# Kernel optimization log

Measured on AMD Instinct MI355X. Metric: run time of the kernel, lower is better.

The kernel has to match this reference:

```python
import jax, jax.numpy as jnp
import numpy as np

N, M, D = 1024, 1024, 512


def setup_inputs() -> dict:
    key = jax.random.key(0)
    ks = jax.random.split(key, 12)
    s = 1.0 / np.sqrt(D)
    return {
        "q": jax.random.normal(ks[0], (N, D), jnp.float32),
        "k": jax.random.normal(ks[1], (M, D), jnp.float32),
        "v": jax.random.normal(ks[2], (M, D), jnp.float32),
        "mask": jax.random.randint(ks[3], (N, M), 0, 2) > 0,
        "Wq": jax.random.normal(ks[4], (D, D), jnp.float32) * s,
        "bq": jax.random.normal(ks[5], (D,), jnp.float32) * s,
        "Wk": jax.random.normal(ks[6], (D, D), jnp.float32) * s,
        "bk": jax.random.normal(ks[7], (D,), jnp.float32) * s,
        "Wv": jax.random.normal(ks[8], (D, D), jnp.float32) * s,
        "bv": jax.random.normal(ks[9], (D,), jnp.float32) * s,
        "Ww": jax.random.normal(ks[10], (D,), jnp.float32) * s,
        "bw": jax.random.normal(ks[11], (1,), jnp.float32) * s,
    }


def reference(q, k, v, mask, Wq, bq, Wk, bk, Wv, bv, Ww, bw):
    # Linear projections (torch Linear: x @ W.T + b)
    qp = q @ Wq.T + bq  # [N, D]
    kp = k @ Wk.T + bk  # [M, D]
    vp = v @ Wv.T + bv  # [M, D]
    # Bahdanau additive score: W(tanh(q_n + k_m)) -> [N, M]
    h = jnp.tanh(qp[:, None, :] + kp[None, :, :])  # [N, M, D]
    scores = jnp.einsum('nmd,d->nm', h, Ww) + bw[0]
    scores = jnp.where(mask, scores, jnp.float32(-1000000.0))
    attn = jax.nn.softmax(scores, axis=1)  # softmax over M (dim 1)
    context = jnp.einsum('nm,md->nd', attn, vp)  # [N, D]
    return context
```

## Files before the change

### kernel.cpp

```cpp
#include <hip/hip_runtime.h>
#include <hip/hip_bf16.h>
#include <float.h>


#define NROWS 1024
#define DDIM  512
#define MDIM  1024

typedef __attribute__((ext_vector_type(8))) short s8v;
typedef __attribute__((ext_vector_type(4))) float f4v;
typedef __attribute__((ext_vector_type(2))) float v2f;

__device__ __forceinline__ ushort f2bf(float f) {
    unsigned u = __float_as_uint(f);
    u = u + 0x7FFFu + ((u >> 16) & 1u);
    return (ushort)(u >> 16);
}
__device__ __forceinline__ float bf2f(ushort h) {
    return __uint_as_float(((unsigned)h) << 16);
}

__device__ __forceinline__ void load_lds16(const float* g, float* l) {
    __builtin_amdgcn_global_load_lds(
        (const __attribute__((address_space(1))) void*)g,
        (__attribute__((address_space(3))) void*)l, 16, 0, 0);
}

__global__ __launch_bounds__(256) void proj_gemm(
    const float* __restrict__ q, const float* __restrict__ kk_,
    const float* __restrict__ v,
    const float* __restrict__ Wq, const float* __restrict__ bq,
    const float* __restrict__ Wk, const float* __restrict__ bk,
    const float* __restrict__ Wv, const float* __restrict__ bv,
    float* __restrict__ eq, float* __restrict__ ekT,
    ushort* __restrict__ vph, ushort* __restrict__ vpl,
    float* __restrict__ rsum, float CS)
{
    __shared__ ushort Ah[4096], Al[4096], Bh[4096], Bl[4096];

    const float* A; const float* B; const float* bias;
    int biasRow;
    if (blockIdx.z == 0)      { A = q;   B = Wq;  bias = bq; biasRow = 0; }
    else if (blockIdx.z == 1) { A = Wk;  B = kk_; bias = bk; biasRow = 1; }
    else                      { A = Wv;  B = v;   bias = bv; biasRow = 1; }

    const int bi = (blockIdx.z == 0) ? blockIdx.x : blockIdx.y;
    const int bj = (blockIdx.z == 0) ? blockIdx.y : blockIdx.x;

    const int t    = threadIdx.x;
    const int lane = t & 63;
    const int w    = t >> 6;
    const int lm   = lane & 15;
    const int lq   = lane >> 4;
    const int i0   = bi * 64;
    const int j0   = bj * 64;
    const int mh   = (w >> 1) * 32;
    const int nh   = (w & 1) * 32;

    if (blockIdx.z == 0 && bi == 0 && bj == 0) {
        float4 zz = {0.f, 0.f, 0.f, 0.f};
        *(float4*)&rsum[t * 4] = zz;
    }

    f4v acc[2][2] = {{{0.f,0.f,0.f,0.f},{0.f,0.f,0.f,0.f}},
                     {{0.f,0.f,0.f,0.f},{0.f,0.f,0.f,0.f}}};
    float4 pa[4], pb[4];

    const int sr = t >> 4, sc4 = t & 15;
#pragma unroll
    for (int p = 0; p < 4; ++p) {
        int r = sr + p * 16;
        pa[p] = *(const float4*)&A[(size_t)(i0 + r) * DDIM + sc4 * 4];
        pb[p] = *(const float4*)&B[(size_t)(j0 + r) * DDIM + sc4 * 4];
    }

    for (int kc = 0; kc < 8; ++kc) {
        __syncthreads();
#pragma unroll
        for (int p = 0; p < 4; ++p) {
            int r = sr + p * 16;
            int ad = r * 64 + (((sc4 >> 1) ^ (r & 7)) << 3) + (sc4 & 1) * 4;
            float af[4] = {pa[p].x, pa[p].y, pa[p].z, pa[p].w};
            float bf[4] = {pb[p].x, pb[p].y, pb[p].z, pb[p].w};
            ushort ah4[4], al4[4], bh4[4], bl4[4];
#pragma unroll
            for (int e = 0; e < 4; ++e) {
                ah4[e] = f2bf(af[e]); al4[e] = f2bf(af[e] - bf2f(ah4[e]));
                bh4[e] = f2bf(bf[e]); bl4[e] = f2bf(bf[e] - bf2f(bh4[e]));
            }
            *(ushort4*)&Ah[ad] = *(ushort4*)ah4;
            *(ushort4*)&Al[ad] = *(ushort4*)al4;
            *(ushort4*)&Bh[ad] = *(ushort4*)bh4;
            *(ushort4*)&Bl[ad] = *(ushort4*)bl4;
        }
        __syncthreads();
        if (kc < 7) {
            const int k0 = (kc + 1) * 64;
#pragma unroll
            for (int p = 0; p < 4; ++p) {
                int r = sr + p * 16;
                pa[p] = *(const float4*)&A[(size_t)(i0 + r) * DDIM + k0 + sc4 * 4];
                pb[p] = *(const float4*)&B[(size_t)(j0 + r) * DDIM + k0 + sc4 * 4];
            }
        }
#pragma unroll
        for (int ks = 0; ks < 2; ++ks) {
            const int kb = ks * 4 + lq;
            s8v afh[2], afl[2], bfh[2], bfl[2];
#pragma unroll
            for (int g = 0; g < 2; ++g) {
                int ra = mh + g * 16 + lm;
                int rb = nh + g * 16 + lm;
                int aa = ra * 64 + ((kb ^ (ra & 7)) << 3);
                int ab = rb * 64 + ((kb ^ (rb & 7)) << 3);
                afh[g] = *(const s8v*)&Ah[aa];
                afl[g] = *(const s8v*)&Al[aa];
                bfh[g] = *(const s8v*)&Bh[ab];
                bfl[g] = *(const s8v*)&Bl[ab];
            }
#pragma unroll
            for (int mi = 0; mi < 2; ++mi)
#pragma unroll
                for (int ni = 0; ni < 2; ++ni) {
                    acc[mi][ni] = __builtin_amdgcn_mfma_f32_16x16x32_bf16(
                        afh[mi], bfh[ni], acc[mi][ni], 0, 0, 0);
                    acc[mi][ni] = __builtin_amdgcn_mfma_f32_16x16x32_bf16(
                        afh[mi], bfl[ni], acc[mi][ni], 0, 0, 0);
                    acc[mi][ni] = __builtin_amdgcn_mfma_f32_16x16x32_bf16(
                        afl[mi], bfh[ni], acc[mi][ni], 0, 0, 0);
                }
        }
    }

    const float CLAMP = 8192.0f;
#pragma unroll
    for (int mi = 0; mi < 2; ++mi) {
#pragma unroll
        for (int ni = 0; ni < 2; ++ni) {
#pragma unroll
            for (int p = 0; p < 4; ++p) {
                int row = i0 + mh + mi * 16 + lq * 4 + p;
                int col = j0 + nh + ni * 16 + lm;
                float val = acc[mi][ni][p] + (biasRow ? bias[row] : bias[col]);
                if (blockIdx.z == 0) {
                    eq[(size_t)row * 512 + col] =
                        fminf(__builtin_amdgcn_exp2f(val * CS), CLAMP);
                } else if (blockIdx.z == 1) {
                    ekT[(size_t)row * 1024 + col] =
                        fminf(__builtin_amdgcn_exp2f(val * CS), CLAMP);
                } else {
                    ushort h = f2bf(val);
                    vph[(size_t)row * 1024 + col] = h;
                    vpl[(size_t)row * 1024 + col] = f2bf(val - bf2f(h));
                }
            }
        }
    }
}

#define DCH  32
#define SMCH 128
__global__ __launch_bounds__(256) void score_kernel(const float* __restrict__ eq,
                                                    const float* __restrict__ ekT,
                                                    const float* __restrict__ Ww,
                                                    const int* __restrict__ mask,
                                                    ushort* __restrict__ Ph,
                                                    ushort* __restrict__ Pl,
                                                    float* __restrict__ rsum)
{
    __shared__ __align__(16) float ks[DCH * SMCH];
    __shared__ __align__(16) float es[16 * DCH];
    __shared__ __align__(16) float wws[DCH];
    const int t    = threadIdx.x;
    const int lane = t & 63;
    const int w    = t >> 6;
    const int m0   = blockIdx.x * SMCH;
    const int n0   = blockIdx.y * 16;

    v2f acc[4] = {};
    const v2f one2 = {1.f, 1.f};

    for (int d0 = 0; d0 < DDIM; d0 += DCH) {
        __syncthreads();
#pragma unroll
        for (int i = 0; i < 4; ++i) {
            int r2 = w * 8 + i * 2;
            const float* g = ekT + (size_t)(d0 + r2 + (lane >> 5)) * MDIM
                             + m0 + (lane & 31) * 4;
            load_lds16(g, &ks[r2 * SMCH]);
        }
#pragma unroll
        for (int p = 0; p < 2; ++p) {
            int idx = t + p * 256;
            int nl = idx >> 5, dd = idx & 31;
            es[nl * DCH + dd] = eq[(size_t)(n0 + nl) * DDIM + d0 + dd];
        }
        if (t < DCH) wws[t] = Ww[d0 + t];
        __syncthreads();

#pragma unroll
        for (int dq = 0; dq < DCH; dq += 4) {
            v2f k0 = *(const v2f*)&ks[(dq + 0) * SMCH + lane * 2];
            v2f k1 = *(const v2f*)&ks[(dq + 1) * SMCH + lane * 2];
            v2f k2 = *(const v2f*)&ks[(dq + 2) * SMCH + lane * 2];
            v2f k3 = *(const v2f*)&ks[(dq + 3) * SMCH + lane * 2];
            float4 wg = *(const float4*)&wws[dq];
#pragma unroll
            for (int nn = 0; nn < 4; ++nn) {
                float4 eg = *(const float4*)&es[(w * 4 + nn) * DCH + dq];
                v2f A0 = __builtin_elementwise_fma(k0, (v2f){eg.x, eg.x}, one2);
                v2f A1 = __builtin_elementwise_fma(k1, (v2f){eg.y, eg.y}, one2);
                v2f A2 = __builtin_elementwise_fma(k2, (v2f){eg.z, eg.z}, one2);
                v2f A3 = __builtin_elementwise_fma(k3, (v2f){eg.w, eg.w}, one2);
                v2f n01 = __builtin_elementwise_fma((v2f){wg.y, wg.y}, A0,
                                                    (v2f){wg.x, wg.x} * A1);
                v2f d01 = A0 * A1;
                v2f n23 = __builtin_elementwise_fma((v2f){wg.w, wg.w}, A2,
                                                    (v2f){wg.z, wg.z} * A3);
                v2f d23 = A2 * A3;
                v2f num = __builtin_elementwise_fma(n01, d23, n23 * d01);
                v2f den = d01 * d23;
                v2f r = {__builtin_amdgcn_rcpf(den.x), __builtin_amdgcn_rcpf(den.y)};
                acc[nn] = __builtin_elementwise_fma(num, r, acc[nn]);
            }
        }
    }

    const float C2 = -2.8853900817779268f;
    const int m = m0 + lane * 2;
#pragma unroll
    for (int nn = 0; nn < 4; ++nn) {
        int n = n0 + w * 4 + nn;
        int2 mk = *(const int2*)&mask[(size_t)n * MDIM + m];
        float o0 = mk.x ? __builtin_amdgcn_exp2f(acc[nn].x * C2) : 0.f;
        float o1 = mk.y ? __builtin_amdgcn_exp2f(acc[nn].y * C2) : 0.f;
        ushort h0 = f2bf(o0), h1 = f2bf(o1);
        ushort l0 = f2bf(o0 - bf2f(h0)), l1 = f2bf(o1 - bf2f(h1));
        ushort2 hh = {h0, h1}, ll = {l0, l1};
        *(ushort2*)&Ph[(size_t)n * MDIM + m] = hh;
        *(ushort2*)&Pl[(size_t)n * MDIM + m] = ll;
        float rs = o0 + o1;
#pragma unroll
        for (int off = 32; off; off >>= 1) rs += __shfl_xor(rs, off);
        if (lane == 0) atomicAdd(&rsum[n], rs);
    }
}

__global__ __launch_bounds__(256) void ctx_gemm(const ushort* __restrict__ Ph,
                                                const ushort* __restrict__ Pl,
                                                const ushort* __restrict__ vph,
                                                const ushort* __restrict__ vpl,
                                                const float* __restrict__ rsum,
                                                float* __restrict__ out)
{
    const int t    = threadIdx.x;
    const int lane = t & 63;
    const int w    = t >> 6;
    const int lm   = lane & 15;
    const int lq   = lane >> 4;
    const int d0   = blockIdx.x * 64 + w * 16;
    const int n0   = blockIdx.y * 16;

    const ushort* pAh = Ph  + (size_t)(n0 + lm) * MDIM + lq * 8;
    const ushort* pAl = Pl  + (size_t)(n0 + lm) * MDIM + lq * 8;
    const ushort* pBh = vph + (size_t)(d0 + lm) * MDIM + lq * 8;
    const ushort* pBl = vpl + (size_t)(d0 + lm) * MDIM + lq * 8;

    f4v acc = {0.f, 0.f, 0.f, 0.f};
#pragma unroll 4
    for (int m0 = 0; m0 < MDIM; m0 += 32) {
        s8v ah = *(const s8v*)(pAh + m0);
        s8v al = *(const s8v*)(pAl + m0);
        s8v bh = *(const s8v*)(pBh + m0);
        s8v bl = *(const s8v*)(pBl + m0);
        acc = __builtin_amdgcn_mfma_f32_16x16x32_bf16(ah, bh, acc, 0, 0, 0);
        acc = __builtin_amdgcn_mfma_f32_16x16x32_bf16(ah, bl, acc, 0, 0, 0);
        acc = __builtin_amdgcn_mfma_f32_16x16x32_bf16(al, bh, acc, 0, 0, 0);
    }

#pragma unroll
    for (int p = 0; p < 4; ++p) {
        int nrow = n0 + lq * 4 + p;
        float inv = __builtin_amdgcn_rcpf(rsum[nrow]);
        out[(size_t)nrow * DDIM + d0 + lm] = acc[p] * inv;
    }
}

extern "C" void kernel_launch(void* const* d_in, const int* in_sizes, int n_in,
                              void* d_out, int out_size, void* d_ws, size_t ws_size,
                              hipStream_t stream)
{
    const float* q    = (const float*)d_in[0];
    const float* k    = (const float*)d_in[1];
    const float* v    = (const float*)d_in[2];
    const int*   mask = (const int*)d_in[3];
    const float* Wq   = (const float*)d_in[4];
    const float* bq   = (const float*)d_in[5];
    const float* Wk   = (const float*)d_in[6];
    const float* bk   = (const float*)d_in[7];
    const float* Wv   = (const float*)d_in[8];
    const float* bv   = (const float*)d_in[9];
    const float* Ww   = (const float*)d_in[10];

    float* ws    = (float*)d_ws;
    float* eq    = ws;
    float* ekT   = ws + 524288;
    ushort* vph  = (ushort*)(ws + 1048576);
    ushort* vpl  = (ushort*)(ws + 1310720);
    ushort* Ph   = (ushort*)(ws + 1572864);
    ushort* Pl   = (ushort*)(ws + 2097152);
    float* rsum  = ws + 2621440;
    float* out   = (float*)d_out;

    const float CS = 2.8853900817779268f;

    proj_gemm<<<dim3(16, 8, 3), dim3(256), 0, stream>>>(q, k, v, Wq, bq, Wk, bk,
                                                        Wv, bv, eq, ekT,
                                                        vph, vpl, rsum, CS);
    score_kernel<<<dim3(8, 64), dim3(256), 0, stream>>>(eq, ekT, Ww, mask,
                                                        Ph, Pl, rsum);
    ctx_gemm<<<dim3(8, 64), dim3(256), 0, stream>>>(Ph, Pl, vph, vpl, rsum, out);
}
```

Baseline: 182.9 us.

## Split score reduction over D across two blocks with atomic partial sums

```diff
diff --git a/kernel.cpp b/kernel.cpp
--- a/kernel.cpp
+++ b/kernel.cpp
@@ -34,7 +34,7 @@
     const float* __restrict__ Wv, const float* __restrict__ bv,
     float* __restrict__ eq, float* __restrict__ ekT,
     ushort* __restrict__ vph, ushort* __restrict__ vpl,
-    float* __restrict__ rsum, float CS)
+    float* __restrict__ S, float CS)
 {
     __shared__ ushort Ah[4096], Al[4096], Bh[4096], Bl[4096];
 
@@ -57,9 +57,12 @@
     const int mh   = (w >> 1) * 32;
     const int nh   = (w & 1) * 32;
 
-    if (blockIdx.z == 0 && bi == 0 && bj == 0) {
+    if (blockIdx.z == 0) {
+        const int jb = blockIdx.x * 8 + blockIdx.y;
         float4 zz = {0.f, 0.f, 0.f, 0.f};
-        *(float4*)&rsum[t * 4] = zz;
+#pragma unroll
+        for (int p = 0; p < 8; ++p)
+            *(float4*)&S[(size_t)jb * 8192 + (t + p * 256) * 4] = zz;
     }
 
     f4v acc[2][2] = {{{0.f,0.f,0.f,0.f},{0.f,0.f,0.f,0.f}},
@@ -163,10 +166,7 @@
 __global__ __launch_bounds__(256) void score_kernel(const float* __restrict__ eq,
                                                     const float* __restrict__ ekT,
                                                     const float* __restrict__ Ww,
-                                                    const int* __restrict__ mask,
-                                                    ushort* __restrict__ Ph,
-                                                    ushort* __restrict__ Pl,
-                                                    float* __restrict__ rsum)
+                                                    float* __restrict__ S)
 {
     __shared__ __align__(16) float ks[DCH * SMCH];
     __shared__ __align__(16) float es[16 * DCH];
@@ -176,11 +176,13 @@
     const int w    = t >> 6;
     const int m0   = blockIdx.x * SMCH;
     const int n0   = blockIdx.y * 16;
+    const int dbase = blockIdx.z * 256;
 
     v2f acc[4] = {};
     const v2f one2 = {1.f, 1.f};
 
-    for (int d0 = 0; d0 < DDIM; d0 += DCH) {
+    for (int dc = 0; dc < 256; dc += DCH) {
+        const int d0 = dbase + dc;
         __syncthreads();
 #pragma unroll
         for (int i = 0; i < 4; ++i) {
@@ -231,19 +233,40 @@
 #pragma unroll
     for (int nn = 0; nn < 4; ++nn) {
         int n = n0 + w * 4 + nn;
-        int2 mk = *(const int2*)&mask[(size_t)n * MDIM + m];
-        float o0 = mk.x ? __builtin_amdgcn_exp2f(acc[nn].x * C2) : 0.f;
-        float o1 = mk.y ? __builtin_amdgcn_exp2f(acc[nn].y * C2) : 0.f;
-        ushort h0 = f2bf(o0), h1 = f2bf(o1);
-        ushort l0 = f2bf(o0 - bf2f(h0)), l1 = f2bf(o1 - bf2f(h1));
-        ushort2 hh = {h0, h1}, ll = {l0, l1};
-        *(ushort2*)&Ph[(size_t)n * MDIM + m] = hh;
-        *(ushort2*)&Pl[(size_t)n * MDIM + m] = ll;
-        float rs = o0 + o1;
-#pragma unroll
-        for (int off = 32; off; off >>= 1) rs += __shfl_xor(rs, off);
-        if (lane == 0) atomicAdd(&rsum[n], rs);
-    }
+        atomicAdd(&S[(size_t)n * MDIM + m],     acc[nn].x * C2);
+        atomicAdd(&S[(size_t)n * MDIM + m + 1], acc[nn].y * C2);
+    }
+}
+
+__global__ __launch_bounds__(256) void combine_kernel(const float* __restrict__ S,
+                                                      const int* __restrict__ mask,
+                                                      ushort* __restrict__ Ph,
+                                                      ushort* __restrict__ Pl,
+                                                      float* __restrict__ rsum)
+{
+    __shared__ float red[4];
+    const int n = blockIdx.x, t = threadIdx.x;
+    const int lane = t & 63, w = t >> 6;
+
+    float4 s  = *(const float4*)&S[(size_t)n * MDIM + t * 4];
+    int4   mk = *(const int4*)&mask[(size_t)n * MDIM + t * 4];
+    float p0 = mk.x ? __builtin_amdgcn_exp2f(s.x) : 0.f;
+    float p1 = mk.y ? __builtin_amdgcn_exp2f(s.y) : 0.f;
+    float p2 = mk.z ? __builtin_amdgcn_exp2f(s.z) : 0.f;
+    float p3 = mk.w ? __builtin_amdgcn_exp2f(s.w) : 0.f;
+
+    ushort h[4] = {f2bf(p0), f2bf(p1), f2bf(p2), f2bf(p3)};
+    ushort l[4] = {f2bf(p0 - bf2f(h[0])), f2bf(p1 - bf2f(h[1])),
+                   f2bf(p2 - bf2f(h[2])), f2bf(p3 - bf2f(h[3]))};
+    *(ushort4*)&Ph[(size_t)n * MDIM + t * 4] = *(ushort4*)h;
+    *(ushort4*)&Pl[(size_t)n * MDIM + t * 4] = *(ushort4*)l;
+
+    float rs = (p0 + p1) + (p2 + p3);
+#pragma unroll
+    for (int off = 32; off; off >>= 1) rs += __shfl_xor(rs, off);
+    if (lane == 0) red[w] = rs;
+    __syncthreads();
+    if (t == 0) rsum[n] = (red[0] + red[1]) + (red[2] + red[3]);
 }
 
 __global__ __launch_bounds__(256) void ctx_gemm(const ushort* __restrict__ Ph,
@@ -307,17 +330,18 @@
     float* ekT   = ws + 524288;
     ushort* vph  = (ushort*)(ws + 1048576);
     ushort* vpl  = (ushort*)(ws + 1310720);
-    ushort* Ph   = (ushort*)(ws + 1572864);
-    ushort* Pl   = (ushort*)(ws + 2097152);
+    float* S     = ws + 1572864;
     float* rsum  = ws + 2621440;
+    ushort* Ph   = (ushort*)ws;
+    ushort* Pl   = (ushort*)(ws + 524288);
     float* out   = (float*)d_out;
 
     const float CS = 2.8853900817779268f;
 
     proj_gemm<<<dim3(16, 8, 3), dim3(256), 0, stream>>>(q, k, v, Wq, bq, Wk, bk,
                                                         Wv, bv, eq, ekT,
-                                                        vph, vpl, rsum, CS);
-    score_kernel<<<dim3(8, 64), dim3(256), 0, stream>>>(eq, ekT, Ww, mask,
-                                                        Ph, Pl, rsum);
+                                                        vph, vpl, S, CS);
+    score_kernel<<<dim3(8, 64, 2), dim3(256), 0, stream>>>(eq, ekT, Ww, S);
+    combine_kernel<<<dim3(1024), dim3(256), 0, stream>>>(S, mask, Ph, Pl, rsum);
     ctx_gemm<<<dim3(8, 64), dim3(256), 0, stream>>>(Ph, Pl, vph, vpl, rsum, out);
 }
```

New measurement: 181.4 us. No clear change (-0.9%).
